# Performance work log

Hardware: AMD Instinct MI355X
Metric: run time of the kernel (lower is better)

## Reference

```python
import jax, jax.numpy as jnp
import numpy as np

N_NODES = 50000
N_EDGES = 800000
INDIM = 128
HIDIM = 128
OUTDIM = 128


def setup_inputs() -> dict:
    key = jax.random.key(0)
    ks = jax.random.split(key, 12)
    x = jax.random.normal(ks[0], (N_NODES, INDIM), dtype=jnp.float32)
    edge_index = jax.random.randint(ks[1], (2, N_EDGES), 0, N_NODES, dtype=jnp.int64)
    edge_weights = jax.random.normal(ks[2], (N_EDGES, 1), dtype=jnp.float32)
    # GINEConv internal edge projection Linear(1 -> feat_dim) per layer
    We1 = jax.random.normal(ks[3], (1, INDIM), dtype=jnp.float32)
    be1 = jnp.zeros((INDIM,), dtype=jnp.float32)
    # layer MLPs (nn.Linear)
    W1 = jax.random.normal(ks[4], (INDIM, HIDIM), dtype=jnp.float32) / np.sqrt(INDIM)
    b1 = jnp.zeros((HIDIM,), dtype=jnp.float32)
    We2 = jax.random.normal(ks[5], (1, HIDIM), dtype=jnp.float32)
    be2 = jnp.zeros((HIDIM,), dtype=jnp.float32)
    W2 = jax.random.normal(ks[6], (HIDIM, OUTDIM), dtype=jnp.float32) / np.sqrt(HIDIM)
    b2 = jnp.zeros((OUTDIM,), dtype=jnp.float32)
    return {"x": x, "edge_index": edge_index, "edge_weights": edge_weights,
            "We1": We1, "be1": be1, "W1": W1, "b1": b1,
            "We2": We2, "be2": be2, "W2": W2, "b2": b2}


def _gine_conv(h, src, dst, edge_attr, We, be, W, b):
    # edge embedding: Linear(1 -> d)
    e = edge_attr @ We + be                     # [E, d]
    # message: relu(x_j + e_ij), gather from source nodes
    msg = jax.nn.relu(h[src] + e)               # [E, d]
    # scatter-sum aggregate at destination nodes
    agg = jax.ops.segment_sum(msg, dst, num_segments=N_NODES)  # [N, d]
    # (1 + eps) * x + aggr, eps = 0 (PyG default), then nn (Linear)
    return (h + agg) @ W + b


def reference(x, edge_index, edge_weights, We1, be1, W1, b1, We2, be2, W2, b2):
    src = edge_index[0]
    dst = edge_index[1]
    h = jax.nn.relu(_gine_conv(x, src, dst, edge_weights, We1, be1, W1, b1))
    out = _gine_conv(h, src, dst, edge_weights, We2, be2, W2, b2)
    return out
```

## Files before the change

kernel.cpp:

```cpp
#include <hip/hip_runtime.h>


typedef unsigned long long u64;
typedef unsigned int u32;
typedef unsigned short ushort;
typedef __attribute__((ext_vector_type(8))) short short8;
typedef __attribute__((ext_vector_type(4))) float f32x4;
typedef __attribute__((ext_vector_type(4))) u32 u32x4;

constexpr int NN = 50000;
constexpr int NE = 800000;
constexpr int D  = 128;
constexpr int BSH = 6;
constexpr int NB  = (NN + 63) >> BSH;
constexpr int NC  = 128;
constexpr int CHUNK = NE / NC;
constexpr int BCAP = 4096;
constexpr int GR = 64;
constexpr int GG = (NN + GR - 1) / GR;
constexpr int CBLK = NN * D / 8 / 256;

__device__ __forceinline__ ushort f2bf(float f) {
    u32 u = __float_as_uint(f);
    return (ushort)((u + 0x7FFFu + ((u >> 16) & 1u)) >> 16);
}
__device__ __forceinline__ float bfl(u32 u) {
    return __uint_as_float(u << 16);
}
__device__ __forceinline__ float bfh(u32 u) {
    return __uint_as_float(u & 0xFFFF0000u);
}
__device__ __forceinline__ u64 pack_edge(int src, int d6, float w) {
    return ((u64)__float_as_uint(w) << 32) | (u32)(src | (d6 << 17));
}


__global__ __launch_bounds__(256) void prep_hist(
    const float* __restrict__ x,  ushort* __restrict__ xb,
    const float* __restrict__ W1, const float* __restrict__ W2,
    ushort* __restrict__ Wt1, ushort* __restrict__ Wt2,
    const int* __restrict__ dst, int* __restrict__ G)
{
    int blk = blockIdx.x;
    if (blk < CBLK) {
        int base = (blk * 256 + threadIdx.x) * 8;
        float4 a = *(const float4*)(x + base);
        float4 b = *(const float4*)(x + base + 4);
        uint4 o;
        o.x = (u32)f2bf(a.x) | ((u32)f2bf(a.y) << 16);
        o.y = (u32)f2bf(a.z) | ((u32)f2bf(a.w) << 16);
        o.z = (u32)f2bf(b.x) | ((u32)f2bf(b.y) << 16);
        o.w = (u32)f2bf(b.z) | ((u32)f2bf(b.w) << 16);
        *(uint4*)(xb + base) = o;
    } else if (blk < CBLK + 8) {
        int b = blk - CBLK;
        const float* W  = (b >= 4) ? W2 : W1;
        ushort*      Wt = (b >= 4) ? Wt2 : Wt1;
        int k0 = (b & 3) * 32;
        for (int i = threadIdx.x; i < 32 * D; i += 256) {
            int n = i >> 5, r = i & 31;
            Wt[n * D + k0 + r] = f2bf(W[(k0 + r) * D + n]);
        }
    } else {
        __shared__ int hh[NB];
        int t = threadIdx.x, c = blk - CBLK - 8;
        for (int i = t; i < NB; i += 256) hh[i] = 0;
        __syncthreads();
        int e0 = c * CHUNK;
        for (int i = t; i < CHUNK; i += 256)
            atomicAdd(&hh[dst[e0 + i] >> BSH], 1);
        __syncthreads();
        for (int i = t; i < NB; i += 256) G[c * NB + i] = hh[i];
    }
}


__global__ __launch_bounds__(1024) void bucket_scatter(
    const int*   __restrict__ src,
    const int*   __restrict__ dst,
    const float* __restrict__ ew,
    const int*   __restrict__ G,
    int*         __restrict__ B,
    u64*         __restrict__ stage)
{
    __shared__ int base_s[NB];
    __shared__ int cnt_s[NB];
    __shared__ int pre_s[NB];
    __shared__ int tsum[1024];
    const int t = threadIdx.x, c = blockIdx.x;

    int S = 0, P = 0;
    if (t < NB) {
        #pragma unroll 8
        for (int cc = 0; cc < NC; ++cc) {
            int g = G[cc * NB + t];
            S += g;
            if (cc < c) P += g;
        }
        pre_s[t] = P;
    }
    tsum[t] = S;
    __syncthreads();

    for (int d = 1; d < 1024; d <<= 1) {
        int v = (t >= d) ? tsum[t - d] : 0;
        __syncthreads();
        tsum[t] += v;
        __syncthreads();
    }
    if (t < NB) base_s[t] = tsum[t] - S;
    __syncthreads();

    if (c == 0) {
        if (t < NB) B[t] = base_s[t];
        if (t == 0) B[NB] = NE;
    }
    if (t < NB) {
        base_s[t] += pre_s[t];
        cnt_s[t] = 0;
    }
    __syncthreads();

    int e0 = c * CHUNK;
    for (int i = t; i < CHUNK; i += 1024) {
        int e  = e0 + i;
        int d  = dst[e];
        int bk = d >> BSH;
        int r  = atomicAdd(&cnt_s[bk], 1);
        stage[base_s[bk] + r] = pack_edge(src[e], d & 63, ew[e]);
    }
}

__global__ __launch_bounds__(256) void bucket_csr(
    const int* __restrict__ B, u64* __restrict__ stage, int* __restrict__ off)
{
    __shared__ u64 buf[BCAP];
    __shared__ int cnt[64];
    __shared__ int cur[64];
    __shared__ int noff[64];
    int t = threadIdx.x, b = blockIdx.x;
    int e0 = B[b], e1 = B[b + 1];
    int n = e1 - e0;
    if (n > BCAP) n = BCAP;
    if (t < 64) { cnt[t] = 0; cur[t] = 0; }
    __syncthreads();
    for (int i = t; i < n; i += 256)
        atomicAdd(&cnt[(int)((stage[e0 + i] >> 17) & 63)], 1);
    __syncthreads();
    if (t == 0) {
        int run = 0;
        for (int j = 0; j < 64; ++j) { noff[j] = run; run += cnt[j]; }
    }
    __syncthreads();
    int n0 = b << BSH;
    if (t < 64 && (n0 + t) < NN) off[n0 + t] = e0 + noff[t];
    if (b == NB - 1 && t == 0) off[NN] = NE;
    for (int i = t; i < n; i += 256) {
        u64 p = stage[e0 + i];
        int d6 = (int)((p >> 17) & 63);
        int r = atomicAdd(&cur[d6], 1);
        buf[noff[d6] + r] = p;
    }
    __syncthreads();
    for (int i = t; i < n; i += 256) stage[e0 + i] = buf[i];
}


__global__ __launch_bounds__(256) void aggregate(
    const ushort* __restrict__ hb,
    const int*    __restrict__ off,
    const u64*    __restrict__ epk,
    const float*  __restrict__ We,
    const float*  __restrict__ be,
    ushort*       __restrict__ aggb)
{
    int tid = blockIdx.x * 256 + threadIdx.x;
    int n = tid >> 4;
    if (n >= NN) return;
    int d8 = (tid & 15) << 3;

    float4 wv0 = *(const float4*)(We + d8);
    float4 wv1 = *(const float4*)(We + d8 + 4);
    float4 bv0 = *(const float4*)(be + d8);
    float4 bv1 = *(const float4*)(be + d8 + 4);

    int e0 = off[n], e1 = off[n + 1];
    float a0=0.f,a1=0.f,a2=0.f,a3=0.f,a4=0.f,a5=0.f,a6=0.f,a7=0.f;

    for (int e = e0; e < e1; e += 8) {
        int m = e1 - e; if (m > 8) m = 8;
        u64 p[8];
        #pragma unroll
        for (int k = 0; k < 8; ++k) p[k] = (k < m) ? epk[e + k] : 0;
        u32x4 hv[8];
        #pragma unroll
        for (int k = 0; k < 8; ++k)
            hv[k] = *(const u32x4*)(hb + (size_t)(p[k] & 0x1FFFF) * D + d8);
        #pragma unroll
        for (int k = 0; k < 8; ++k) {
            if (k < m) {
                float w = __uint_as_float((u32)(p[k] >> 32));
                a0 += fmaxf(0.f, bfl(hv[k].x) + fmaf(w, wv0.x, bv0.x));
                a1 += fmaxf(0.f, bfh(hv[k].x) + fmaf(w, wv0.y, bv0.y));
                a2 += fmaxf(0.f, bfl(hv[k].y) + fmaf(w, wv0.z, bv0.z));
                a3 += fmaxf(0.f, bfh(hv[k].y) + fmaf(w, wv0.w, bv0.w));
                a4 += fmaxf(0.f, bfl(hv[k].z) + fmaf(w, wv1.x, bv1.x));
                a5 += fmaxf(0.f, bfh(hv[k].z) + fmaf(w, wv1.y, bv1.y));
                a6 += fmaxf(0.f, bfl(hv[k].w) + fmaf(w, wv1.z, bv1.z));
                a7 += fmaxf(0.f, bfh(hv[k].w) + fmaf(w, wv1.w, bv1.w));
            }
        }
    }
    u32x4 o;
    o.x = (u32)f2bf(a0) | ((u32)f2bf(a1) << 16);
    o.y = (u32)f2bf(a2) | ((u32)f2bf(a3) << 16);
    o.z = (u32)f2bf(a4) | ((u32)f2bf(a5) << 16);
    o.w = (u32)f2bf(a6) | ((u32)f2bf(a7) << 16);
    __builtin_nontemporal_store(o, (u32x4*)(aggb + (size_t)n * D + d8));
}


__global__ __launch_bounds__(256) void gemm_mfma(
    const ushort* __restrict__ A1b,
    const ushort* __restrict__ A2b,
    const ushort* __restrict__ Wtb,
    const float*  __restrict__ bias,
    float*        __restrict__ outf,
    ushort*       __restrict__ outb,
    int relu)
{
    __shared__ ushort As[GR * 140];
    __shared__ ushort Ws[D * 140];

    const int t    = threadIdx.x;
    const int row0 = blockIdx.x * GR;

    for (int c = t; c < GR * (D / 4); c += 256) {
        int r  = c >> 5;
        int k4 = (c & 31) << 2;
        int row = row0 + r;
        uint2 o = make_uint2(0u, 0u);
        if (row < NN) {
            uint2 u1 = *(const uint2*)(A1b + (size_t)row * D + k4);
            u64 uu = __builtin_nontemporal_load((const u64*)(A2b + (size_t)row * D + k4));
            uint2 u2 = make_uint2((u32)uu, (u32)(uu >> 32));
            float s0 = bfl(u1.x) + bfl(u2.x);
            float s1 = bfh(u1.x) + bfh(u2.x);
            float s2 = bfl(u1.y) + bfl(u2.y);
            float s3 = bfh(u1.y) + bfh(u2.y);
            o.x = (u32)f2bf(s0) | ((u32)f2bf(s1) << 16);
            o.y = (u32)f2bf(s2) | ((u32)f2bf(s3) << 16);
        }
        *(uint2*)&As[r * 140 + k4] = o;
    }
    for (int c = t; c < D * (D / 4); c += 256) {
        int r  = c >> 5;
        int k4 = (c & 31) << 2;
        *(uint2*)&Ws[r * 140 + k4] = *(const uint2*)(Wtb + r * D + k4);
    }
    __syncthreads();

    const int wave = t >> 6;
    const int lane = t & 63;
    const int q    = lane >> 4;
    const int m    = lane & 15;
    const int wr   = (wave >> 1) * 32;
    const int wc   = (wave & 1) * 64;

    f32x4 acc[2][4] = {};
    #pragma unroll
    for (int kb = 0; kb < 4; ++kb) {
        int ak = kb * 32 + q * 8;
        short8 af[2];
        #pragma unroll
        for (int rg = 0; rg < 2; ++rg)
            af[rg] = *(const short8*)&As[(wr + rg * 16 + m) * 140 + ak];
        #pragma unroll
        for (int ct = 0; ct < 4; ++ct) {
            short8 bf = *(const short8*)&Ws[(wc + ct * 16 + m) * 140 + ak];
            #pragma unroll
            for (int rg = 0; rg < 2; ++rg)
                acc[rg][ct] = __builtin_amdgcn_mfma_f32_16x16x32_bf16(
                    af[rg], bf, acc[rg][ct], 0, 0, 0);
        }
    }

    #pragma unroll
    for (int ct = 0; ct < 4; ++ct) {
        int col = wc + ct * 16 + m;
        float bc = bias[col];
        #pragma unroll
        for (int rg = 0; rg < 2; ++rg) {
            #pragma unroll
            for (int r = 0; r < 4; ++r) {
                int grow = row0 + wr + rg * 16 + q * 4 + r;
                if (grow < NN) {
                    float v = acc[rg][ct][r] + bc;
                    if (relu) v = fmaxf(0.f, v);
                    if (outb) outb[(size_t)grow * D + col] = f2bf(v);
                    else __builtin_nontemporal_store(v, outf + (size_t)grow * D + col);
                }
            }
        }
    }
}

extern "C" void kernel_launch(void* const* d_in, const int* in_sizes, int n_in,
                              void* d_out, int out_size, void* d_ws, size_t ws_size,
                              hipStream_t stream)
{
    const float* x   = (const float*)d_in[0];
    const int*   ei  = (const int*)  d_in[1];
    const float* ew  = (const float*)d_in[2];
    const float* We1 = (const float*)d_in[3];
    const float* be1 = (const float*)d_in[4];
    const float* W1  = (const float*)d_in[5];
    const float* b1  = (const float*)d_in[6];
    const float* We2 = (const float*)d_in[7];
    const float* be2 = (const float*)d_in[8];
    const float* W2  = (const float*)d_in[9];
    const float* b2  = (const float*)d_in[10];

    float* out = (float*)d_out;

    ushort* xb   = (ushort*)d_ws;
    ushort* hb   = xb + (size_t)NN * D;
    ushort* aggb = hb + (size_t)NN * D;
    ushort* Wt1  = aggb + (size_t)NN * D;
    ushort* Wt2  = Wt1 + D * D;
    u64*   stage = (u64*)(Wt2 + D * D);
    int*   G     = (int*)(stage + NE);
    int*   B     = G + NC * NB;
    int*   off   = B + NB + 2;

    const int* src = ei;
    const int* dst = ei + NE;

    dim3 agrid((NN * 16 + 255) / 256);

    prep_hist<<<CBLK + 8 + NC, 256, 0, stream>>>(x, xb, W1, W2, Wt1, Wt2,
                                                 dst, G);

    bucket_scatter<<<NC, 1024, 0, stream>>>(src, dst, ew, G, B, stage);
    bucket_csr<<<NB, 256, 0, stream>>>(B, stage, off);

    aggregate<<<agrid, 256, 0, stream>>>(xb, off, stage, We1, be1, aggb);
    gemm_mfma<<<GG, 256, 0, stream>>>(xb, aggb, Wt1, b1, nullptr, hb, 1);

    aggregate<<<agrid, 256, 0, stream>>>(hb, off, stage, We2, be2, aggb);
    gemm_mfma<<<GG, 256, 0, stream>>>(hb, aggb, Wt2, b2, out, nullptr, 0);
}
```

Measured before the change: 255.6 us.

## Fuse neighbor aggregation into MFMA GEMM kernel per GINE layer

Merges the edge aggregation kernel into the GEMM kernel so each block aggregates its 64 rows directly into shared memory, adding the self term in fp32 before a single bf16 rounding. This removes the intermediate aggregation buffer write/read and one kernel launch per layer. In exchange, the gather phase now runs inside large-LDS blocks with fewer resident waves, which may reduce latency hiding for the random gathers.

Result: slower. 262.0 us (+2.5%).

```diff
diff --git a/kernel.cpp b/kernel.cpp
--- a/kernel.cpp
+++ b/kernel.cpp
@@ -166,63 +166,12 @@
 }
 
 
-__global__ __launch_bounds__(256) void aggregate(
+__global__ __launch_bounds__(256) void gine_layer(
     const ushort* __restrict__ hb,
     const int*    __restrict__ off,
     const u64*    __restrict__ epk,
     const float*  __restrict__ We,
     const float*  __restrict__ be,
-    ushort*       __restrict__ aggb)
-{
-    int tid = blockIdx.x * 256 + threadIdx.x;
-    int n = tid >> 4;
-    if (n >= NN) return;
-    int d8 = (tid & 15) << 3;
-
-    float4 wv0 = *(const float4*)(We + d8);
-    float4 wv1 = *(const float4*)(We + d8 + 4);
-    float4 bv0 = *(const float4*)(be + d8);
-    float4 bv1 = *(const float4*)(be + d8 + 4);
-
-    int e0 = off[n], e1 = off[n + 1];
-    float a0=0.f,a1=0.f,a2=0.f,a3=0.f,a4=0.f,a5=0.f,a6=0.f,a7=0.f;
-
-    for (int e = e0; e < e1; e += 8) {
-        int m = e1 - e; if (m > 8) m = 8;
-        u64 p[8];
-        #pragma unroll
-        for (int k = 0; k < 8; ++k) p[k] = (k < m) ? epk[e + k] : 0;
-        u32x4 hv[8];
-        #pragma unroll
-        for (int k = 0; k < 8; ++k)
-            hv[k] = *(const u32x4*)(hb + (size_t)(p[k] & 0x1FFFF) * D + d8);
-        #pragma unroll
-        for (int k = 0; k < 8; ++k) {
-            if (k < m) {
-                float w = __uint_as_float((u32)(p[k] >> 32));
-                a0 += fmaxf(0.f, bfl(hv[k].x) + fmaf(w, wv0.x, bv0.x));
-                a1 += fmaxf(0.f, bfh(hv[k].x) + fmaf(w, wv0.y, bv0.y));
-                a2 += fmaxf(0.f, bfl(hv[k].y) + fmaf(w, wv0.z, bv0.z));
-                a3 += fmaxf(0.f, bfh(hv[k].y) + fmaf(w, wv0.w, bv0.w));
-                a4 += fmaxf(0.f, bfl(hv[k].z) + fmaf(w, wv1.x, bv1.x));
-                a5 += fmaxf(0.f, bfh(hv[k].z) + fmaf(w, wv1.y, bv1.y));
-                a6 += fmaxf(0.f, bfl(hv[k].w) + fmaf(w, wv1.z, bv1.z));
-                a7 += fmaxf(0.f, bfh(hv[k].w) + fmaf(w, wv1.w, bv1.w));
-            }
-        }
-    }
-    u32x4 o;
-    o.x = (u32)f2bf(a0) | ((u32)f2bf(a1) << 16);
-    o.y = (u32)f2bf(a2) | ((u32)f2bf(a3) << 16);
-    o.z = (u32)f2bf(a4) | ((u32)f2bf(a5) << 16);
-    o.w = (u32)f2bf(a6) | ((u32)f2bf(a7) << 16);
-    __builtin_nontemporal_store(o, (u32x4*)(aggb + (size_t)n * D + d8));
-}
-
-
-__global__ __launch_bounds__(256) void gemm_mfma(
-    const ushort* __restrict__ A1b,
-    const ushort* __restrict__ A2b,
     const ushort* __restrict__ Wtb,
     const float*  __restrict__ bias,
     float*        __restrict__ outf,
@@ -235,28 +184,63 @@
     const int t    = threadIdx.x;
     const int row0 = blockIdx.x * GR;
 
-    for (int c = t; c < GR * (D / 4); c += 256) {
-        int r  = c >> 5;
-        int k4 = (c & 31) << 2;
-        int row = row0 + r;
-        uint2 o = make_uint2(0u, 0u);
-        if (row < NN) {
-            uint2 u1 = *(const uint2*)(A1b + (size_t)row * D + k4);
-            u64 uu = __builtin_nontemporal_load((const u64*)(A2b + (size_t)row * D + k4));
-            uint2 u2 = make_uint2((u32)uu, (u32)(uu >> 32));
-            float s0 = bfl(u1.x) + bfl(u2.x);
-            float s1 = bfh(u1.x) + bfh(u2.x);
-            float s2 = bfl(u1.y) + bfl(u2.y);
-            float s3 = bfh(u1.y) + bfh(u2.y);
-            o.x = (u32)f2bf(s0) | ((u32)f2bf(s1) << 16);
-            o.y = (u32)f2bf(s2) | ((u32)f2bf(s3) << 16);
-        }
-        *(uint2*)&As[r * 140 + k4] = o;
-    }
     for (int c = t; c < D * (D / 4); c += 256) {
         int r  = c >> 5;
         int k4 = (c & 31) << 2;
         *(uint2*)&Ws[r * 140 + k4] = *(const uint2*)(Wtb + r * D + k4);
+    }
+
+    const int g  = t >> 4;
+    const int d8 = (t & 15) << 3;
+
+    float4 wv0 = *(const float4*)(We + d8);
+    float4 wv1 = *(const float4*)(We + d8 + 4);
+    float4 bv0 = *(const float4*)(be + d8);
+    float4 bv1 = *(const float4*)(be + d8 + 4);
+
+    for (int nrep = 0; nrep < 4; ++nrep) {
+        int ln = nrep * 16 + g;
+        int n  = row0 + ln;
+        float a0=0.f,a1=0.f,a2=0.f,a3=0.f,a4=0.f,a5=0.f,a6=0.f,a7=0.f;
+        if (n < NN) {
+            int e0 = off[n], e1 = off[n + 1];
+            for (int e = e0; e < e1; e += 8) {
+                int m = e1 - e; if (m > 8) m = 8;
+                u64 p[8];
+                #pragma unroll
+                for (int k = 0; k < 8; ++k) p[k] = (k < m) ? epk[e + k] : 0;
+                u32x4 hv[8];
+                #pragma unroll
+                for (int k = 0; k < 8; ++k)
+                    hv[k] = *(const u32x4*)(hb + (size_t)(p[k] & 0x1FFFF) * D + d8);
+                #pragma unroll
+                for (int k = 0; k < 8; ++k) {
+                    if (k < m) {
+                        float w = __uint_as_float((u32)(p[k] >> 32));
+                        a0 += fmaxf(0.f, bfl(hv[k].x) + fmaf(w, wv0.x, bv0.x));
+                        a1 += fmaxf(0.f, bfh(hv[k].x) + fmaf(w, wv0.y, bv0.y));
+                        a2 += fmaxf(0.f, bfl(hv[k].y) + fmaf(w, wv0.z, bv0.z));
+                        a3 += fmaxf(0.f, bfh(hv[k].y) + fmaf(w, wv0.w, bv0.w));
+                        a4 += fmaxf(0.f, bfl(hv[k].z) + fmaf(w, wv1.x, bv1.x));
+                        a5 += fmaxf(0.f, bfh(hv[k].z) + fmaf(w, wv1.y, bv1.y));
+                        a6 += fmaxf(0.f, bfl(hv[k].w) + fmaf(w, wv1.z, bv1.z));
+                        a7 += fmaxf(0.f, bfh(hv[k].w) + fmaf(w, wv1.w, bv1.w));
+                    }
+                }
+            }
+            u32x4 sv = *(const u32x4*)(hb + (size_t)n * D + d8);
+            a0 += bfl(sv.x); a1 += bfh(sv.x);
+            a2 += bfl(sv.y); a3 += bfh(sv.y);
+            a4 += bfl(sv.z); a5 += bfh(sv.z);
+            a6 += bfl(sv.w); a7 += bfh(sv.w);
+        }
+        uint2 lo, hi;
+        lo.x = (u32)f2bf(a0) | ((u32)f2bf(a1) << 16);
+        lo.y = (u32)f2bf(a2) | ((u32)f2bf(a3) << 16);
+        hi.x = (u32)f2bf(a4) | ((u32)f2bf(a5) << 16);
+        hi.y = (u32)f2bf(a6) | ((u32)f2bf(a7) << 16);
+        *(uint2*)&As[ln * 140 + d8]     = lo;
+        *(uint2*)&As[ln * 140 + d8 + 4] = hi;
     }
     __syncthreads();
 
@@ -336,17 +320,15 @@
     const int* src = ei;
     const int* dst = ei + NE;
 
-    dim3 agrid((NN * 16 + 255) / 256);
-
     prep_hist<<<CBLK + 8 + NC, 256, 0, stream>>>(x, xb, W1, W2, Wt1, Wt2,
                                                  dst, G);
 
     bucket_scatter<<<NC, 1024, 0, stream>>>(src, dst, ew, G, B, stage);
     bucket_csr<<<NB, 256, 0, stream>>>(B, stage, off);
 
-    aggregate<<<agrid, 256, 0, stream>>>(xb, off, stage, We1, be1, aggb);
-    gemm_mfma<<<GG, 256, 0, stream>>>(xb, aggb, Wt1, b1, nullptr, hb, 1);
-
-    aggregate<<<agrid, 256, 0, stream>>>(hb, off, stage, We2, be2, aggb);
-    gemm_mfma<<<GG, 256, 0, stream>>>(hb, aggb, Wt2, b2, out, nullptr, 0);
-}
+    gine_layer<<<GG, 256, 0, stream>>>(xb, off, stage, We1, be1, Wt1, b1,
+                                       nullptr, hb, 1);
+
+    gine_layer<<<GG, 256, 0, stream>>>(hb, off, stage, We2, be2, Wt2, b2,
+                                       out, nullptr, 0);
+}
```
